# Optimization experiments

Hardware: AMD Instinct MI355X
Metric: run time of the kernel (lower is better)

## Reference

```python
import jax, jax.numpy as jnp
import numpy as np

# static config matching init_kwargs / setup
T = 0.1      # temperature
MARG = 0.0   # margin m
NEG_IOU = 0.5
K = 1        # pos_topk
WEIGHT = 1.0
P = 2080     # number of True entries in mask2d (triu of 64x64)


def _normalize(x, axis=-1, eps=1e-12):
    n = jnp.sqrt(jnp.sum(x * x, axis=axis, keepdims=True))
    return x / jnp.maximum(n, eps)


def _log_ce(pos_scores, all_scores, neg_mask, t, m):
    # pos_scores: (..., K); all_scores: (..., K or 1, L); neg_mask broadcastable to all_scores
    pos_logit = (pos_scores - m) / t
    pos_exp = jnp.exp(pos_logit)
    neg_exp_sum = jnp.sum(jnp.exp(all_scores / t) * neg_mask.astype(all_scores.dtype), axis=-1)
    loss = -(pos_logit - jnp.log(pos_exp + neg_exp_sum))
    return jnp.mean(loss)


def setup_inputs() -> dict:
    key = jax.random.key(0)
    k1, k2, k3, k4 = jax.random.split(key, 4)
    S, C, N, B, M = 64, 256, 64, 16, 128
    video_feats = jax.random.normal(k1, (S, C, N, N), dtype=jnp.float32)
    sents_feats = jax.random.normal(k2, (S, C), dtype=jnp.float32)
    iou2d = jax.random.uniform(k3, (S, N, N), dtype=jnp.float32)
    iou2ds = jax.random.uniform(k4, (M, N, N), dtype=jnp.float32)
    num_sentences = jnp.full((B,), 4, dtype=jnp.int32)   # sum == S
    num_targets = jnp.full((S,), 2, dtype=jnp.int32)     # sum == M
    mask2d = jnp.triu(jnp.ones((N, N), dtype=bool))      # P = 2080 valid proposals
    return {
        "video_feats": video_feats, "sents_feats": sents_feats,
        "iou2d": iou2d, "iou2ds": iou2ds,
        "num_sentences": num_sentences, "num_targets": num_targets,
        "mask2d": mask2d,
    }


def reference(video_feats, sents_feats, iou2d, iou2ds, num_sentences, num_targets, mask2d):
    S, C, N, _ = video_feats.shape
    B = num_sentences.shape[0]
    M = iou2ds.shape[0]

    # flat proposal indices (static count P)
    mask_idx = jnp.nonzero(mask2d.reshape(-1), size=P)[0]

    # scatter maps
    scatter_b2s = jnp.concatenate([jnp.zeros((1,), jnp.int32),
                                   jnp.cumsum(num_sentences)[:-1].astype(jnp.int32)])  # (B,)
    scatter_m2s = jnp.repeat(jnp.arange(S), num_targets, total_repeat_length=M)        # (M,)
    scatter_s2b = jnp.repeat(jnp.arange(B), num_sentences, total_repeat_length=S)      # (S,)

    # select valid proposals: (S,C,P) -> (S,P,C)
    vf = video_feats.reshape(S, C, N * N)[:, :, mask_idx].transpose(0, 2, 1)
    iou2d_f = iou2d.reshape(S, N * N)[:, mask_idx]    # (S,P)
    iou2ds_f = iou2ds.reshape(M, N * N)[:, mask_idx]  # (M,P)

    vf = _normalize(vf, axis=-1)          # (S,P,C)
    sf = _normalize(sents_feats, axis=-1) # (S,C)

    # top-K proposals per moment
    topk_idxs = jax.lax.top_k(iou2ds_f, K)[1]                         # (M,K)
    allm_vf = vf[scatter_m2s]                                         # (M,P,C)
    topk_vf = jnp.take_along_axis(allm_vf, topk_idxs[:, :, None], 1)  # (M,K,C)

    # inter-video loss
    inter_video_pos = jnp.sum(topk_vf * sf[scatter_m2s][:, None, :], axis=-1)  # (M,K)
    inter_video_all = jnp.einsum('mkc,sc->mks', topk_vf, sf)                   # (M,K,S)
    eye_mask = ~jnp.eye(S, dtype=bool)
    inter_video_neg_mask = eye_mask[scatter_m2s][:, None, :]                   # (M,1,S)
    loss_inter_video = _log_ce(inter_video_pos, inter_video_all, inter_video_neg_mask, T, MARG)

    # inter-query loss
    inter_query_pos = inter_video_pos                                  # (M,K)
    vf_b = vf[scatter_b2s].reshape(B * P, C)                           # one sentence-rep per video
    inter_query_all = jnp.einsum('sc,qc->sq', sf, vf_b)[:, None, :]    # (S,1,B*P)

    # pos_mask: row s has its video block b=scatter_s2b[s] set to (iou2d > neg_iou)
    s2v_pos = iou2d_f > NEG_IOU                                        # (S,P)
    pos_mask = jnp.zeros((S, B, P), dtype=bool)
    pos_mask = pos_mask.at[jnp.arange(S), scatter_s2b].set(s2v_pos)
    pos_mask = pos_mask.reshape(S, B * P)
    inter_query_neg_mask = (~pos_mask)[:, None, :]                     # (S,1,B*P)

    loss_inter_query = _log_ce(inter_query_pos,
                               inter_query_all[scatter_m2s],
                               inter_query_neg_mask[scatter_m2s], T, MARG)

    return (loss_inter_video + loss_inter_query) * WEIGHT
```

## Files before the change

kernel.cpp:

```cpp
#include <hip/hip_runtime.h>
#include <math.h>

#define C 256
#define NLEN 64
#define NN 4096
#define T_INV 10.0f
#define NEG_IOU_TH 0.5f
#define SGROUP 16
#define FLATS 2

__device__ __forceinline__ float wave_reduce_sum(float v) {
    #pragma unroll
    for (int off = 32; off > 0; off >>= 1) v += __shfl_xor(v, off, 64);
    return v;
}

__global__ void k_scatter(const int* __restrict__ num_sentences,
                          const int* __restrict__ num_targets,
                          int B, int S, int M,
                          int* __restrict__ b2s, int* __restrict__ s2b,
                          int* __restrict__ m2s, float* __restrict__ denomq) {
    if (threadIdx.x == 0) {
        int acc = 0;
        for (int b = 0; b < B; ++b) {
            b2s[b] = acc;
            int ns = num_sentences[b];
            for (int k = 0; k < ns; ++k) s2b[acc + k] = b;
            acc += ns;
        }
        int mi = 0;
        for (int s = 0; s < S; ++s) {
            int nt = num_targets[s];
            for (int k = 0; k < nt; ++k) m2s[mi++] = s;
        }
    }
    for (int i = threadIdx.x; i < S; i += blockDim.x) denomq[i] = 0.f;
}

__global__ void k_norm_sf(const float* __restrict__ sents,
                          float* __restrict__ sfT, int S) {
    __shared__ float red[4];
    int s = blockIdx.x, tid = threadIdx.x;
    float v = sents[(size_t)s * C + tid];
    float ss = wave_reduce_sum(v * v);
    int lane = tid & 63, wave = tid >> 6;
    if (lane == 0) red[wave] = ss;
    __syncthreads();
    float tot = red[0] + red[1] + red[2] + red[3];
    float inv = 1.0f / fmaxf(sqrtf(tot), 1e-12f);
    sfT[(size_t)tid * S + s] = v * inv;
}

__global__ void k_topk(const float* __restrict__ vf,
                       const float* __restrict__ iou2ds,
                       const float* __restrict__ sfT,
                       const int* __restrict__ m2s,
                       float* __restrict__ pos, float* __restrict__ negiv,
                       int S) {
    __shared__ float tv[C];
    __shared__ float sred[4];
    __shared__ int   sidx[4];
    __shared__ float sc4[4][64];
    __shared__ int   bestflat;
    int m = blockIdx.x, tid = threadIdx.x;
    int s_m = m2s[m];
    int lane = tid & 63, wave = tid >> 6;

    float bv = -1e30f; int bi = NN;
    #pragma unroll
    for (int j = 0; j < NN / 256; ++j) {
        int flat = tid + j * 256;
        int r = flat >> 6, cc = flat & 63;
        if (cc >= r) {
            float val = iou2ds[(size_t)m * NN + flat];
            if (val > bv || (val == bv && flat < bi)) { bv = val; bi = flat; }
        }
    }
    #pragma unroll
    for (int off = 32; off > 0; off >>= 1) {
        float ov = __shfl_xor(bv, off, 64);
        int   oi = __shfl_xor(bi, off, 64);
        if (ov > bv || (ov == bv && oi < bi)) { bv = ov; bi = oi; }
    }
    if (lane == 0) { sred[wave] = bv; sidx[wave] = bi; }
    __syncthreads();
    if (tid == 0) {
        float v0 = sred[0]; int i0 = sidx[0];
        for (int w = 1; w < 4; ++w)
            if (sred[w] > v0 || (sred[w] == v0 && sidx[w] < i0)) { v0 = sred[w]; i0 = sidx[w]; }
        bestflat = i0;
    }
    __syncthreads();
    int flat = bestflat;

    float v = vf[((size_t)s_m * C + tid) * NN + flat];
    float ss = wave_reduce_sum(v * v);
    if (lane == 0) sred[wave] = ss;
    __syncthreads();
    float tot = sred[0] + sred[1] + sred[2] + sred[3];
    float inv = 1.0f / fmaxf(sqrtf(tot), 1e-12f);
    tv[tid] = v * inv;
    __syncthreads();

    {
        int s = tid & 63, cg = tid >> 6;
        float d = 0.f;
        for (int j = 0; j < 64; ++j) {
            int c2 = cg * 64 + j;
            d += tv[c2] * sfT[(size_t)c2 * S + s];
        }
        sc4[cg][s] = d;
    }
    __syncthreads();
    if (tid < 64) {
        float d = sc4[0][tid] + sc4[1][tid] + sc4[2][tid] + sc4[3][tid];
        if (tid == s_m) pos[m] = d;
        float e = (tid == s_m) ? 0.f : expf(d * T_INV);
        e = wave_reduce_sum(e);
        if (tid == 0) negiv[m] = e;
    }
}

__global__ void __launch_bounds__(256)
k_q(const float* __restrict__ vf, const float* __restrict__ iou2d,
    const float* __restrict__ sfT, const int* __restrict__ b2s,
    const int* __restrict__ num_sentences,
    float* __restrict__ denomq, int S) {
    __shared__ float sT[C * SGROUP];
    __shared__ float dw[4][SGROUP];
    int tile = blockIdx.x, b = blockIdx.y, g = blockIdx.z;
    int tid = threadIdx.x;
    int sb = b2s[b];
    int ns = num_sentences[b];
    int s0 = g * SGROUP;

    for (int k = tid; k < C * SGROUP; k += 256) {
        int c = k >> 4, s = k & (SGROUP - 1);
        sT[k] = sfT[(size_t)c * S + s0 + s];
    }
    __syncthreads();

    int flat0 = tile * (256 * FLATS) + tid * FLATS;
    const float2* vp = (const float2*)(vf + (size_t)sb * C * NN + flat0);

    float acc0[SGROUP], acc1[SGROUP];
    #pragma unroll
    for (int s = 0; s < SGROUP; ++s) { acc0[s] = 0.f; acc1[s] = 0.f; }
    float ss0 = 0.f, ss1 = 0.f;

    #pragma unroll 2
    for (int c = 0; c < C; ++c) {
        float2 v = vp[(size_t)c * (NN / 2)];
        ss0 += v.x * v.x;
        ss1 += v.y * v.y;
        const float4* sr = (const float4*)&sT[c * SGROUP];
        #pragma unroll
        for (int q = 0; q < SGROUP / 4; ++q) {
            float4 s4 = sr[q];
            acc0[q*4+0] += s4.x * v.x;  acc1[q*4+0] += s4.x * v.y;
            acc0[q*4+1] += s4.y * v.x;  acc1[q*4+1] += s4.y * v.y;
            acc0[q*4+2] += s4.z * v.x;  acc1[q*4+2] += s4.z * v.y;
            acc0[q*4+3] += s4.w * v.x;  acc1[q*4+3] += s4.w * v.y;
        }
    }

    int fA = flat0, fB = flat0 + 1;
    bool vA = ((fA & 63) >= (fA >> 6));
    bool vB = ((fB & 63) >= (fB >> 6));
    float invA = 1.0f / fmaxf(sqrtf(ss0), 1e-12f);
    float invB = 1.0f / fmaxf(sqrtf(ss1), 1e-12f);

    unsigned long long bitsA = 0ull, bitsB = 0ull;
    for (int i = 0; i < ns; ++i) {
        const float* row = iou2d + (size_t)(sb + i) * NN;
        if (vA && row[fA] > NEG_IOU_TH) bitsA |= (1ull << i);
        if (vB && row[fB] > NEG_IOU_TH) bitsB |= (1ull << i);
    }

    int lane = tid & 63, wave = tid >> 6;
    #pragma unroll
    for (int s = 0; s < SGROUP; ++s) {
        int s_abs = s0 + s;
        int rel = s_abs - sb;
        bool inblk = (rel >= 0 && rel < ns);
        float e = 0.f;
        if (vA && !(inblk && ((bitsA >> rel) & 1ull)))
            e += expf(acc0[s] * invA * T_INV);
        if (vB && !(inblk && ((bitsB >> rel) & 1ull)))
            e += expf(acc1[s] * invB * T_INV);
        e = wave_reduce_sum(e);
        if (lane == 0) dw[wave][s] = e;
    }
    __syncthreads();
    if (tid < SGROUP) {
        float tot = dw[0][tid] + dw[1][tid] + dw[2][tid] + dw[3][tid];
        atomicAdd(&denomq[s0 + tid], tot);
    }
}

__global__ void k_final(const float* __restrict__ pos,
                        const float* __restrict__ negiv,
                        const float* __restrict__ denomq,
                        const int* __restrict__ m2s,
                        float* __restrict__ out, int M) {
    __shared__ float red[2];
    int tid = threadIdx.x;
    float val = 0.f;
    if (tid < M) {
        int s = m2s[tid];
        float pl = pos[tid] * T_INV;
        float pe = expf(pl);
        float liv = -(pl - logf(pe + negiv[tid]));
        float liq = -(pl - logf(pe + denomq[s]));
        val = liv + liq;
    }
    val = wave_reduce_sum(val);
    int lane = tid & 63, wave = tid >> 6;
    if (lane == 0) red[wave] = val;
    __syncthreads();
    if (tid == 0) out[0] = (red[0] + red[1]) / (float)M;
}

extern "C" void kernel_launch(void* const* d_in, const int* in_sizes, int n_in,
                              void* d_out, int out_size, void* d_ws, size_t ws_size,
                              hipStream_t stream) {
    const float* video_feats   = (const float*)d_in[0];
    const float* sents_feats   = (const float*)d_in[1];
    const float* iou2d         = (const float*)d_in[2];
    const float* iou2ds        = (const float*)d_in[3];
    const int*   num_sentences = (const int*)d_in[4];
    const int*   num_targets   = (const int*)d_in[5];

    const int S = in_sizes[2] / NN;
    const int B = in_sizes[4];
    const int M = in_sizes[3] / NN;

    float* sfT    = (float*)d_ws;
    float* pos    = sfT + (size_t)C * 64;
    float* negiv  = pos + M;
    float* denomq = negiv + M;
    int*   b2s    = (int*)(denomq + S);
    int*   s2b    = b2s + B;
    int*   m2s    = s2b + S;

    k_scatter<<<1, 64, 0, stream>>>(num_sentences, num_targets, B, S, M,
                                    b2s, s2b, m2s, denomq);
    k_norm_sf<<<S, C, 0, stream>>>(sents_feats, sfT, S);
    k_topk<<<M, 256, 0, stream>>>(video_feats, iou2ds, sfT, m2s, pos, negiv, S);
    k_q<<<dim3(NN / (256 * FLATS), B, S / SGROUP), 256, 0, stream>>>(
        video_feats, iou2d, sfT, b2s, num_sentences, denomq, S);
    k_final<<<1, 128, 0, stream>>>(pos, negiv, denomq, m2s, (float*)d_out, M);
}
```

Baseline: 415.6 us.

## Fuse kernels into prep plus main kernel with last-block finalize

Merges the scatter and sentence-normalisation kernels into one prep kernel. The top-k and query-denominator kernels become one heterogeneous grid, and the final reduction runs in the last block to finish, detected with an atomic counter. SGROUP rises from 16 to 32, so each block reuses each video-feature load across twice as many sentences and the grid halves. The goal is fewer launches and less redundant reading of video features, at the cost of more accumulator registers and possibly lower occupancy.

```diff
diff --git a/kernel.cpp b/kernel.cpp
--- a/kernel.cpp
+++ b/kernel.cpp
@@ -2,12 +2,12 @@
 #include <math.h>
 
 #define C 256
-#define NLEN 64
 #define NN 4096
 #define T_INV 10.0f
 #define NEG_IOU_TH 0.5f
-#define SGROUP 16
+#define SGROUP 32
 #define FLATS 2
+#define QTILES (NN / (256 * FLATS))
 
 __device__ __forceinline__ float wave_reduce_sum(float v) {
     #pragma unroll
@@ -15,210 +15,213 @@
     return v;
 }
 
-__global__ void k_scatter(const int* __restrict__ num_sentences,
-                          const int* __restrict__ num_targets,
-                          int B, int S, int M,
-                          int* __restrict__ b2s, int* __restrict__ s2b,
-                          int* __restrict__ m2s, float* __restrict__ denomq) {
-    if (threadIdx.x == 0) {
-        int acc = 0;
-        for (int b = 0; b < B; ++b) {
-            b2s[b] = acc;
-            int ns = num_sentences[b];
-            for (int k = 0; k < ns; ++k) s2b[acc + k] = b;
-            acc += ns;
-        }
-        int mi = 0;
-        for (int s = 0; s < S; ++s) {
-            int nt = num_targets[s];
-            for (int k = 0; k < nt; ++k) m2s[mi++] = s;
-        }
-    }
-    for (int i = threadIdx.x; i < S; i += blockDim.x) denomq[i] = 0.f;
-}
-
-__global__ void k_norm_sf(const float* __restrict__ sents,
-                          float* __restrict__ sfT, int S) {
+__global__ void k_prep(const float* __restrict__ sents,
+                       const int* __restrict__ num_sentences,
+                       const int* __restrict__ num_targets,
+                       int B, int S, int M,
+                       float* __restrict__ sfT, int* __restrict__ b2s,
+                       int* __restrict__ s2b, int* __restrict__ m2s,
+                       float* __restrict__ denomq, int* __restrict__ counter) {
     __shared__ float red[4];
     int s = blockIdx.x, tid = threadIdx.x;
     float v = sents[(size_t)s * C + tid];
-    float ss = wave_reduce_sum(v * v);
+    float ssq = wave_reduce_sum(v * v);
     int lane = tid & 63, wave = tid >> 6;
-    if (lane == 0) red[wave] = ss;
+    if (lane == 0) red[wave] = ssq;
     __syncthreads();
     float tot = red[0] + red[1] + red[2] + red[3];
-    float inv = 1.0f / fmaxf(sqrtf(tot), 1e-12f);
-    sfT[(size_t)tid * S + s] = v * inv;
-}
-
-__global__ void k_topk(const float* __restrict__ vf,
-                       const float* __restrict__ iou2ds,
-                       const float* __restrict__ sfT,
-                       const int* __restrict__ m2s,
-                       float* __restrict__ pos, float* __restrict__ negiv,
-                       int S) {
-    __shared__ float tv[C];
-    __shared__ float sred[4];
+    sfT[(size_t)tid * S + s] = v * (1.0f / fmaxf(sqrtf(tot), 1e-12f));
+
+    if (blockIdx.x == 0) {
+        if (tid < S) denomq[tid] = 0.f;
+        if (tid == 0) {
+            *counter = 0;
+            int acc = 0;
+            for (int b = 0; b < B; ++b) {
+                b2s[b] = acc;
+                int nsb = num_sentences[b];
+                for (int k = 0; k < nsb; ++k) s2b[acc + k] = b;
+                acc += nsb;
+            }
+            int mi = 0;
+            for (int si = 0; si < S; ++si) {
+                int nt = num_targets[si];
+                for (int k = 0; k < nt; ++k) m2s[mi++] = si;
+            }
+        }
+    }
+}
+
+__global__ void __launch_bounds__(256)
+k_main(const float* __restrict__ vf, const float* __restrict__ iou2d,
+       const float* __restrict__ iou2ds, const int* __restrict__ num_sentences,
+       const float* __restrict__ sfT, const int* __restrict__ b2s,
+       const int* __restrict__ m2s,
+       float* __restrict__ pos, float* __restrict__ negiv,
+       float* __restrict__ denomq, int* __restrict__ counter,
+       float* __restrict__ out, int S, int B, int M, int nq, int ntot) {
+    __shared__ float smem[C * SGROUP];
+    __shared__ float red[4];
     __shared__ int   sidx[4];
-    __shared__ float sc4[4][64];
+    __shared__ float dw[4][SGROUP];
     __shared__ int   bestflat;
-    int m = blockIdx.x, tid = threadIdx.x;
-    int s_m = m2s[m];
+    __shared__ int   amlast;
+
+    int bid = blockIdx.x, tid = threadIdx.x;
     int lane = tid & 63, wave = tid >> 6;
 
-    float bv = -1e30f; int bi = NN;
-    #pragma unroll
-    for (int j = 0; j < NN / 256; ++j) {
-        int flat = tid + j * 256;
-        int r = flat >> 6, cc = flat & 63;
-        if (cc >= r) {
-            float val = iou2ds[(size_t)m * NN + flat];
-            if (val > bv || (val == bv && flat < bi)) { bv = val; bi = flat; }
-        }
-    }
-    #pragma unroll
-    for (int off = 32; off > 0; off >>= 1) {
-        float ov = __shfl_xor(bv, off, 64);
-        int   oi = __shfl_xor(bi, off, 64);
-        if (ov > bv || (ov == bv && oi < bi)) { bv = ov; bi = oi; }
-    }
-    if (lane == 0) { sred[wave] = bv; sidx[wave] = bi; }
+    if (bid < nq) {
+        int tile = bid % QTILES;
+        int rem  = bid / QTILES;
+        int b    = rem % B;
+        int g    = rem / B;
+        int sb = b2s[b];
+        int ns = num_sentences[b];
+        int s0 = g * SGROUP;
+
+        for (int k = tid; k < C * SGROUP; k += 256) {
+            int c = k / SGROUP, s = k % SGROUP;
+            smem[k] = sfT[(size_t)c * S + s0 + s];
+        }
+        __syncthreads();
+
+        int flat0 = tile * (256 * FLATS) + tid * FLATS;
+        const float2* vp = (const float2*)(vf + (size_t)sb * C * NN + flat0);
+
+        float2 acc[SGROUP];
+        #pragma unroll
+        for (int s = 0; s < SGROUP; ++s) acc[s] = make_float2(0.f, 0.f);
+        float2 ssq = make_float2(0.f, 0.f);
+
+        #pragma unroll 2
+        for (int c = 0; c < C; ++c) {
+            float2 v = vp[(size_t)c * (NN / 2)];
+            ssq.x += v.x * v.x;
+            ssq.y += v.y * v.y;
+            const float4* sr = (const float4*)&smem[c * SGROUP];
+            #pragma unroll
+            for (int q = 0; q < SGROUP / 4; ++q) {
+                float4 s4 = sr[q];
+                acc[q*4+0].x += s4.x * v.x;  acc[q*4+0].y += s4.x * v.y;
+                acc[q*4+1].x += s4.y * v.x;  acc[q*4+1].y += s4.y * v.y;
+                acc[q*4+2].x += s4.z * v.x;  acc[q*4+2].y += s4.z * v.y;
+                acc[q*4+3].x += s4.w * v.x;  acc[q*4+3].y += s4.w * v.y;
+            }
+        }
+
+        int fA = flat0, fB = flat0 + 1;
+        bool vA = ((fA & 63) >= (fA >> 6));
+        bool vB = ((fB & 63) >= (fB >> 6));
+        float invA = 1.0f / fmaxf(sqrtf(ssq.x), 1e-12f);
+        float invB = 1.0f / fmaxf(sqrtf(ssq.y), 1e-12f);
+
+        unsigned long long bitsA = 0ull, bitsB = 0ull;
+        for (int i = 0; i < ns; ++i) {
+            const float* row = iou2d + (size_t)(sb + i) * NN;
+            if (vA && row[fA] > NEG_IOU_TH) bitsA |= (1ull << i);
+            if (vB && row[fB] > NEG_IOU_TH) bitsB |= (1ull << i);
+        }
+
+        #pragma unroll
+        for (int s = 0; s < SGROUP; ++s) {
+            int s_abs = s0 + s;
+            int rel = s_abs - sb;
+            bool inblk = (rel >= 0 && rel < ns);
+            float e = 0.f;
+            if (vA && !(inblk && ((bitsA >> rel) & 1ull)))
+                e += expf(acc[s].x * invA * T_INV);
+            if (vB && !(inblk && ((bitsB >> rel) & 1ull)))
+                e += expf(acc[s].y * invB * T_INV);
+            e = wave_reduce_sum(e);
+            if (lane == 0) dw[wave][s] = e;
+        }
+        __syncthreads();
+        if (tid < SGROUP)
+            atomicAdd(&denomq[s0 + tid],
+                      dw[0][tid] + dw[1][tid] + dw[2][tid] + dw[3][tid]);
+    } else {
+        int m = bid - nq;
+        int s_m = m2s[m];
+        float* tv  = smem;
+        float* sc4 = smem + C;
+
+        float bv = -1e30f; int bi = NN;
+        #pragma unroll
+        for (int j = 0; j < NN / 256; ++j) {
+            int flat = tid + j * 256;
+            int r = flat >> 6, cc = flat & 63;
+            if (cc >= r) {
+                float val = iou2ds[(size_t)m * NN + flat];
+                if (val > bv || (val == bv && flat < bi)) { bv = val; bi = flat; }
+            }
+        }
+        #pragma unroll
+        for (int off = 32; off > 0; off >>= 1) {
+            float ov = __shfl_xor(bv, off, 64);
+            int   oi = __shfl_xor(bi, off, 64);
+            if (ov > bv || (ov == bv && oi < bi)) { bv = ov; bi = oi; }
+        }
+        if (lane == 0) { red[wave] = bv; sidx[wave] = bi; }
+        __syncthreads();
+        if (tid == 0) {
+            float v0 = red[0]; int i0 = sidx[0];
+            for (int w = 1; w < 4; ++w)
+                if (red[w] > v0 || (red[w] == v0 && sidx[w] < i0)) { v0 = red[w]; i0 = sidx[w]; }
+            bestflat = i0;
+        }
+        __syncthreads();
+        int flat = bestflat;
+
+        float v = vf[((size_t)s_m * C + tid) * NN + flat];
+        float ssq = wave_reduce_sum(v * v);
+        if (lane == 0) red[wave] = ssq;
+        __syncthreads();
+        float tot = red[0] + red[1] + red[2] + red[3];
+        tv[tid] = v * (1.0f / fmaxf(sqrtf(tot), 1e-12f));
+        __syncthreads();
+
+        {
+            int s = tid & 63, cg = tid >> 6;
+            float d = 0.f;
+            for (int j = 0; j < 64; ++j) {
+                int c2 = cg * 64 + j;
+                d += tv[c2] * sfT[(size_t)c2 * S + s];
+            }
+            sc4[cg * 64 + s] = d;
+        }
+        __syncthreads();
+        if (tid < 64) {
+            float d = sc4[tid] + sc4[64 + tid] + sc4[128 + tid] + sc4[192 + tid];
+            if (tid == s_m) atomicExch(&pos[m], d);
+            float e = (tid == s_m) ? 0.f : expf(d * T_INV);
+            e = wave_reduce_sum(e);
+            if (tid == 0) atomicExch(&negiv[m], e);
+        }
+    }
+
     __syncthreads();
     if (tid == 0) {
-        float v0 = sred[0]; int i0 = sidx[0];
-        for (int w = 1; w < 4; ++w)
-            if (sred[w] > v0 || (sred[w] == v0 && sidx[w] < i0)) { v0 = sred[w]; i0 = sidx[w]; }
-        bestflat = i0;
-    }
-    __syncthreads();
-    int flat = bestflat;
-
-    float v = vf[((size_t)s_m * C + tid) * NN + flat];
-    float ss = wave_reduce_sum(v * v);
-    if (lane == 0) sred[wave] = ss;
-    __syncthreads();
-    float tot = sred[0] + sred[1] + sred[2] + sred[3];
-    float inv = 1.0f / fmaxf(sqrtf(tot), 1e-12f);
-    tv[tid] = v * inv;
-    __syncthreads();
-
-    {
-        int s = tid & 63, cg = tid >> 6;
-        float d = 0.f;
-        for (int j = 0; j < 64; ++j) {
-            int c2 = cg * 64 + j;
-            d += tv[c2] * sfT[(size_t)c2 * S + s];
-        }
-        sc4[cg][s] = d;
-    }
-    __syncthreads();
-    if (tid < 64) {
-        float d = sc4[0][tid] + sc4[1][tid] + sc4[2][tid] + sc4[3][tid];
-        if (tid == s_m) pos[m] = d;
-        float e = (tid == s_m) ? 0.f : expf(d * T_INV);
-        e = wave_reduce_sum(e);
-        if (tid == 0) negiv[m] = e;
-    }
-}
-
-__global__ void __launch_bounds__(256)
-k_q(const float* __restrict__ vf, const float* __restrict__ iou2d,
-    const float* __restrict__ sfT, const int* __restrict__ b2s,
-    const int* __restrict__ num_sentences,
-    float* __restrict__ denomq, int S) {
-    __shared__ float sT[C * SGROUP];
-    __shared__ float dw[4][SGROUP];
-    int tile = blockIdx.x, b = blockIdx.y, g = blockIdx.z;
-    int tid = threadIdx.x;
-    int sb = b2s[b];
-    int ns = num_sentences[b];
-    int s0 = g * SGROUP;
-
-    for (int k = tid; k < C * SGROUP; k += 256) {
-        int c = k >> 4, s = k & (SGROUP - 1);
-        sT[k] = sfT[(size_t)c * S + s0 + s];
-    }
-    __syncthreads();
-
-    int flat0 = tile * (256 * FLATS) + tid * FLATS;
-    const float2* vp = (const float2*)(vf + (size_t)sb * C * NN + flat0);
-
-    float acc0[SGROUP], acc1[SGROUP];
-    #pragma unroll
-    for (int s = 0; s < SGROUP; ++s) { acc0[s] = 0.f; acc1[s] = 0.f; }
-    float ss0 = 0.f, ss1 = 0.f;
-
-    #pragma unroll 2
-    for (int c = 0; c < C; ++c) {
-        float2 v = vp[(size_t)c * (NN / 2)];
-        ss0 += v.x * v.x;
-        ss1 += v.y * v.y;
-        const float4* sr = (const float4*)&sT[c * SGROUP];
-        #pragma unroll
-        for (int q = 0; q < SGROUP / 4; ++q) {
-            float4 s4 = sr[q];
-            acc0[q*4+0] += s4.x * v.x;  acc1[q*4+0] += s4.x * v.y;
-            acc0[q*4+1] += s4.y * v.x;  acc1[q*4+1] += s4.y * v.y;
-            acc0[q*4+2] += s4.z * v.x;  acc1[q*4+2] += s4.z * v.y;
-            acc0[q*4+3] += s4.w * v.x;  acc1[q*4+3] += s4.w * v.y;
-        }
-    }
-
-    int fA = flat0, fB = flat0 + 1;
-    bool vA = ((fA & 63) >= (fA >> 6));
-    bool vB = ((fB & 63) >= (fB >> 6));
-    float invA = 1.0f / fmaxf(sqrtf(ss0), 1e-12f);
-    float invB = 1.0f / fmaxf(sqrtf(ss1), 1e-12f);
-
-    unsigned long long bitsA = 0ull, bitsB = 0ull;
-    for (int i = 0; i < ns; ++i) {
-        const float* row = iou2d + (size_t)(sb + i) * NN;
-        if (vA && row[fA] > NEG_IOU_TH) bitsA |= (1ull << i);
-        if (vB && row[fB] > NEG_IOU_TH) bitsB |= (1ull << i);
-    }
-
-    int lane = tid & 63, wave = tid >> 6;
-    #pragma unroll
-    for (int s = 0; s < SGROUP; ++s) {
-        int s_abs = s0 + s;
-        int rel = s_abs - sb;
-        bool inblk = (rel >= 0 && rel < ns);
-        float e = 0.f;
-        if (vA && !(inblk && ((bitsA >> rel) & 1ull)))
-            e += expf(acc0[s] * invA * T_INV);
-        if (vB && !(inblk && ((bitsB >> rel) & 1ull)))
-            e += expf(acc1[s] * invB * T_INV);
-        e = wave_reduce_sum(e);
-        if (lane == 0) dw[wave][s] = e;
-    }
-    __syncthreads();
-    if (tid < SGROUP) {
-        float tot = dw[0][tid] + dw[1][tid] + dw[2][tid] + dw[3][tid];
-        atomicAdd(&denomq[s0 + tid], tot);
-    }
-}
-
-__global__ void k_final(const float* __restrict__ pos,
-                        const float* __restrict__ negiv,
-                        const float* __restrict__ denomq,
-                        const int* __restrict__ m2s,
-                        float* __restrict__ out, int M) {
-    __shared__ float red[2];
-    int tid = threadIdx.x;
+        __threadfence();
+        int old = atomicAdd(counter, 1);
+        amlast = (old == ntot - 1) ? 1 : 0;
+    }
+    __syncthreads();
+    if (!amlast) return;
+
+    __threadfence();
     float val = 0.f;
-    if (tid < M) {
-        int s = m2s[tid];
-        float pl = pos[tid] * T_INV;
+    for (int m = tid; m < M; m += 256) {
+        int s = m2s[m];
+        float pl  = atomicAdd(&pos[m], 0.f) * T_INV;
+        float niv = atomicAdd(&negiv[m], 0.f);
+        float dq  = atomicAdd(&denomq[s], 0.f);
         float pe = expf(pl);
-        float liv = -(pl - logf(pe + negiv[tid]));
-        float liq = -(pl - logf(pe + denomq[s]));
-        val = liv + liq;
+        val += -(pl - logf(pe + niv)) + -(pl - logf(pe + dq));
     }
     val = wave_reduce_sum(val);
-    int lane = tid & 63, wave = tid >> 6;
-    if (lane == 0) red[wave] = val;
-    __syncthreads();
-    if (tid == 0) out[0] = (red[0] + red[1]) / (float)M;
+    if (lane == 0) dw[0][wave] = val;
+    __syncthreads();
+    if (tid == 0) out[0] = (dw[0][0] + dw[0][1] + dw[0][2] + dw[0][3]) / (float)M;
 }
 
 extern "C" void kernel_launch(void* const* d_in, const int* in_sizes, int n_in,
@@ -242,12 +245,14 @@
     int*   b2s    = (int*)(denomq + S);
     int*   s2b    = b2s + B;
     int*   m2s    = s2b + S;
-
-    k_scatter<<<1, 64, 0, stream>>>(num_sentences, num_targets, B, S, M,
-                                    b2s, s2b, m2s, denomq);
-    k_norm_sf<<<S, C, 0, stream>>>(sents_feats, sfT, S);
-    k_topk<<<M, 256, 0, stream>>>(video_feats, iou2ds, sfT, m2s, pos, negiv, S);
-    k_q<<<dim3(NN / (256 * FLATS), B, S / SGROUP), 256, 0, stream>>>(
-        video_feats, iou2d, sfT, b2s, num_sentences, denomq, S);
-    k_final<<<1, 128, 0, stream>>>(pos, negiv, denomq, m2s, (float*)d_out, M);
-}
+    int*   counter = m2s + M;
+
+    const int nq   = QTILES * B * (S / SGROUP);
+    const int ntot = nq + M;
+
+    k_prep<<<S, C, 0, stream>>>(sents_feats, num_sentences, num_targets,
+                                B, S, M, sfT, b2s, s2b, m2s, denomq, counter);
+    k_main<<<ntot, 256, 0, stream>>>(video_feats, iou2d, iou2ds, num_sentences,
+                                     sfT, b2s, m2s, pos, negiv, denomq, counter,
+                                     (float*)d_out, S, B, M, nq, ntot);
+}
```

Result: slower. 469.7 us (+13.0%).
